# Kernel tuning notes

Measured on AMD Instinct MI355X. Metric: run time of the kernel, lower is better.

## Reference

```python
import jax, jax.numpy as jnp
import numpy as np


def setup_inputs() -> dict:
    key = jax.random.key(0)
    ks = jax.random.split(key, 5)
    B, N, d_emb, d_red = 8, 2048, 1024, 512
    x0 = jax.random.normal(ks[0], (B, N, d_emb), dtype=jnp.float32)
    x1 = jax.random.normal(ks[1], (B, N, d_emb), dtype=jnp.float32)
    x2 = jax.random.normal(ks[2], (B, N, d_emb), dtype=jnp.float32)
    Wq = jax.random.normal(ks[3], (d_emb, d_red), dtype=jnp.float32) * (1.0 / np.sqrt(d_emb))
    Wk = jax.random.normal(ks[4], (d_emb, d_red), dtype=jnp.float32) * (1.0 / np.sqrt(d_emb))
    bq = jnp.zeros((d_red,), dtype=jnp.float32)
    bk = jnp.zeros((d_red,), dtype=jnp.float32)
    return {"x0": x0, "x1": x1, "x2": x2, "Wq": Wq, "bq": bq, "Wk": Wk, "bk": bk}


def reference(x0, x1, x2, Wq, bq, Wk, bk):
    d_red = Wq.shape[1]
    # projections; NOTE: original code applies the K projection to x2 (v = self.k(x[2]))
    q = (x0 @ Wq + bq) * (1.0 / np.sqrt(d_red).astype(np.float32))
    k = x1 @ Wk + bk
    v = x2 @ Wk + bk
    scores = jnp.einsum('bqd,bkd->bqk', q, k)  # [B, N, N]
    N = scores.shape[-1]
    row = jnp.arange(N)[:, None]
    col = jnp.arange(N)[None, :]
    causal = jnp.where(col > row, -jnp.inf, 0.0).astype(scores.dtype)
    scores = scores + causal
    attn = jax.nn.softmax(scores, axis=-1)
    return jnp.einsum('bqk,bkd->bqd', attn, v)
```

## Files before the change

### kernel.cpp

```cpp
#include <hip/hip_runtime.h>
#include <hip/hip_bf16.h>
#include <math.h>


typedef __bf16 bf16_t;
typedef __attribute__((ext_vector_type(8))) __bf16 bf16x8;
typedef __attribute__((ext_vector_type(4))) __bf16 bf16x4;
typedef __attribute__((ext_vector_type(4))) float f32x4;

#define MFMA16(a, b, c) __builtin_amdgcn_mfma_f32_16x16x32_bf16((a), (b), (c), 0, 0, 0)

#define XSTR 72

__device__ __forceinline__ void stage16(const void* g, void* l) {
  __builtin_amdgcn_global_load_lds(
      (__attribute__((address_space(1))) void*)(uintptr_t)g,
      (__attribute__((address_space(3))) void*)l, 16, 0, 0);
}

#define PIPE_WAIT_MORE                          \
  {                                             \
    asm volatile("" ::: "memory");              \
    __builtin_amdgcn_s_waitcnt(0x0F74);         \
    __builtin_amdgcn_s_barrier();               \
    asm volatile("" ::: "memory");              \
  }
#define PIPE_WAIT_LAST                          \
  {                                             \
    asm volatile("" ::: "memory");              \
    __builtin_amdgcn_s_waitcnt(0x0F70);         \
    __builtin_amdgcn_s_barrier();               \
    asm volatile("" ::: "memory");              \
  }

#define PROJ_BAR_A                                    \
  {                                                   \
    asm volatile("s_waitcnt lgkmcnt(0)" ::: "memory"); \
    __builtin_amdgcn_s_barrier();                     \
    asm volatile("" ::: "memory");                    \
  }
#define PROJ_BAR_B                                    \
  {                                                   \
    __builtin_amdgcn_sched_barrier(0);                \
    __builtin_amdgcn_s_barrier();                     \
    asm volatile("" ::: "memory");                    \
  }

__global__ __launch_bounds__(256) void wt_kernel(const float* __restrict__ Wq,
                                                 const float* __restrict__ Wk,
                                                 bf16_t* __restrict__ Wtq,
                                                 bf16_t* __restrict__ Wtk) {
  __shared__ float tile[32][33];
  int bid = blockIdx.x;
  int mat = bid >> 9;
  int rem = bid & 511;
  int kt = rem >> 4, nt = rem & 15;
  int k0 = kt * 32, n0 = nt * 32;
  const float* src = mat ? Wk : Wq;
  bf16_t* dst = mat ? Wtk : Wtq;
  int t = threadIdx.x;
  int r = t >> 3, c4 = (t & 7) * 4;
  float4 v = *(const float4*)(src + (k0 + r) * 512 + n0 + c4);
  tile[r][c4 + 0] = v.x; tile[r][c4 + 1] = v.y;
  tile[r][c4 + 2] = v.z; tile[r][c4 + 3] = v.w;
  __syncthreads();
  bf16x4 o;
  o[0] = (bf16_t)tile[c4 + 0][r];
  o[1] = (bf16_t)tile[c4 + 1][r];
  o[2] = (bf16_t)tile[c4 + 2][r];
  o[3] = (bf16_t)tile[c4 + 3][r];
  *(bf16x4*)(dst + (n0 + r) * 1024 + k0 + c4) = o;
}

__global__ __launch_bounds__(256, 3) void proj_kernel(
    const float* __restrict__ x0, const float* __restrict__ x1, const float* __restrict__ x2,
    const bf16_t* __restrict__ Wtq, const bf16_t* __restrict__ Wtk,
    const float* __restrict__ bq, const float* __restrict__ bk,
    bf16_t* __restrict__ qo, bf16_t* __restrict__ ko, bf16_t* __restrict__ vT) {
  __shared__ __align__(16) bf16_t Xs[128 * XSTR];
  __shared__ __align__(16) bf16_t Ws[128 * XSTR];
  int bid = blockIdx.x;
  int xcd = bid & 7;
  int i5 = bid >> 3;
  int nblk = i5 & 3;
  int g = (i5 >> 2) * 8 + xcd;
  int mat = g >> 7;
  int mblk = g & 127;
  const float* xsrc = (mat == 0) ? x0 : ((mat == 1) ? x1 : x2);
  const bf16_t* wsrc = (mat == 0) ? Wtq : Wtk;
  int tid = threadIdx.x;
  int wave = tid >> 6, lane = tid & 63, lhi = lane >> 4, llo = lane & 15;

  f32x4 acc[2][8];
#pragma unroll
  for (int i = 0; i < 2; ++i)
#pragma unroll
    for (int j = 0; j < 8; ++j) acc[i][j] = (f32x4){0.f, 0.f, 0.f, 0.f};

  int xrow = tid >> 1, xseg = tid & 1;
  int wrow = tid >> 1, wseg = tid & 1;
  const float* xbase = xsrc + (size_t)(mblk * 128 + xrow) * 1024 + xseg * 32;
  const bf16_t* wbase = wsrc + (size_t)(nblk * 128 + wrow) * 1024 + wseg * 32;

  float4 nx[8];
  bf16x8 nw[4];

#pragma unroll
  for (int i = 0; i < 8; ++i) nx[i] = *(const float4*)(xbase + i * 4);
#pragma unroll
  for (int i = 0; i < 4; ++i) nw[i] = *(const bf16x8*)(wbase + i * 8);
  {
    bf16_t tmp[32];
#pragma unroll
    for (int i = 0; i < 8; ++i) {
      tmp[i * 4 + 0] = (bf16_t)nx[i].x; tmp[i * 4 + 1] = (bf16_t)nx[i].y;
      tmp[i * 4 + 2] = (bf16_t)nx[i].z; tmp[i * 4 + 3] = (bf16_t)nx[i].w;
    }
#pragma unroll
    for (int i = 0; i < 4; ++i)
      *(bf16x8*)(&Xs[xrow * XSTR + xseg * 32 + i * 8]) = *(bf16x8*)(&tmp[i * 8]);
#pragma unroll
    for (int i = 0; i < 4; ++i)
      *(bf16x8*)(&Ws[wrow * XSTR + wseg * 32 + i * 8]) = nw[i];
  }

  for (int kt = 0; kt < 16; ++kt) {
    PROJ_BAR_A;
    if (kt < 15) {
      int k0 = (kt + 1) * 64;
#pragma unroll
      for (int i = 0; i < 8; ++i) nx[i] = *(const float4*)(xbase + k0 + i * 4);
#pragma unroll
      for (int i = 0; i < 4; ++i) nw[i] = *(const bf16x8*)(wbase + k0 + i * 8);
    }
#pragma unroll
    for (int ks = 0; ks < 2; ++ks) {
      bf16x8 af[2], bfr[8];
#pragma unroll
      for (int mt = 0; mt < 2; ++mt)
        af[mt] = *(const bf16x8*)(&Xs[(wave * 32 + mt * 16 + llo) * XSTR + ks * 32 + lhi * 8]);
#pragma unroll
      for (int nt = 0; nt < 8; ++nt)
        bfr[nt] = *(const bf16x8*)(&Ws[(nt * 16 + llo) * XSTR + ks * 32 + lhi * 8]);
#pragma unroll
      for (int mt = 0; mt < 2; ++mt)
#pragma unroll
        for (int nt = 0; nt < 8; ++nt)
          acc[mt][nt] = MFMA16(af[mt], bfr[nt], acc[mt][nt]);
    }
    if (kt < 15) {
      PROJ_BAR_B;
      bf16_t tmp[32];
#pragma unroll
      for (int i = 0; i < 8; ++i) {
        tmp[i * 4 + 0] = (bf16_t)nx[i].x; tmp[i * 4 + 1] = (bf16_t)nx[i].y;
        tmp[i * 4 + 2] = (bf16_t)nx[i].z; tmp[i * 4 + 3] = (bf16_t)nx[i].w;
      }
#pragma unroll
      for (int i = 0; i < 4; ++i)
        *(bf16x8*)(&Xs[xrow * XSTR + xseg * 32 + i * 8]) = *(bf16x8*)(&tmp[i * 8]);
#pragma unroll
      for (int i = 0; i < 4; ++i)
        *(bf16x8*)(&Ws[wrow * XSTR + wseg * 32 + i * 8]) = nw[i];
    }
  }

  const float* bias = (mat == 0) ? bq : bk;
  float scale = (mat == 0) ? 0.044194173824159216f : 1.0f;
#pragma unroll
  for (int mt = 0; mt < 2; ++mt) {
#pragma unroll
    for (int nt = 0; nt < 8; ++nt) {
      int n = nblk * 128 + nt * 16 + llo;
      float bv = bias[n];
      int rowb = mblk * 128 + wave * 32 + mt * 16 + lhi * 4;
      float vals[4];
#pragma unroll
      for (int r = 0; r < 4; ++r) vals[r] = (acc[mt][nt][r] + bv) * scale;
      if (mat == 0) {
#pragma unroll
        for (int r = 0; r < 4; ++r) qo[(size_t)(rowb + r) * 512 + n] = (bf16_t)vals[r];
      } else if (mat == 1) {
#pragma unroll
        for (int r = 0; r < 4; ++r) ko[(size_t)(rowb + r) * 512 + n] = (bf16_t)vals[r];
      } else {
        int batch = rowb >> 11, tok = rowb & 2047;
        bf16x4 o;
        o[0] = (bf16_t)vals[0]; o[1] = (bf16_t)vals[1];
        o[2] = (bf16_t)vals[2]; o[3] = (bf16_t)vals[3];
        *(bf16x4*)(vT + (size_t)(batch * 512 + n) * 2048 + tok) = o;
      }
    }
  }
}

__device__ __forceinline__ void issueK(const bf16_t* kbase, int key0, int cd,
                                       bf16_t* buf, int wave, int lane) {
#pragma unroll
  for (int i = 0; i < 4; ++i) {
    int idx = wave * 256 + i * 64 + lane;
    int key = idx >> 4, p = idx & 15;
    int s = p ^ (key & 7);
    stage16(kbase + (size_t)(key0 + key) * 512 + cd * 128 + s * 8,
            buf + (size_t)(wave * 256 + i * 64) * 8);
  }
}
__device__ __forceinline__ void issueV(const bf16_t* vbase, int key0, int cv,
                                       bf16_t* buf, int wave, int lane) {
#pragma unroll
  for (int i = 0; i < 4; ++i) {
    int idx = wave * 256 + i * 64 + lane;
    int dl = idx >> 3, p = idx & 7;
    int s = p ^ (dl & 7);
    stage16(vbase + (size_t)(cv * 128 + dl) * 2048 + key0 + s * 8,
            buf + (size_t)(wave * 256 + i * 64) * 8);
  }
}

__global__ __launch_bounds__(256, 2) void attn_kernel(
    const bf16_t* __restrict__ qg, const bf16_t* __restrict__ kg,
    const bf16_t* __restrict__ vTg, float* __restrict__ out,
    bf16_t* __restrict__ Opart, float* __restrict__ msum, float* __restrict__ lsum) {
  __shared__ __align__(16) bf16_t Pipe[3][8192];
  __shared__ __align__(16) bf16_t Plds[4][16 * XSTR];

  int bid = blockIdx.x;
  int b = bid & 7, jj = bid >> 3;
  int t = 31, base = 0, n = 6;
  for (;;) {
    int nt_ = (t + 6) / 6;
    if (jj < base + nt_) { n = nt_; break; }
    base += nt_; --t;
  }
  int c = jj - base;
  int kbs = t + 1;
  int csz = (kbs + n - 1) / n;
  int kb_lo = c * csz;
  int kb_hi = min(kbs, kb_lo + csz);
  int q0 = t * 64;

  int tid = threadIdx.x;
  int wave = tid >> 6, lane = tid & 63, lhi = lane >> 4, llo = lane & 15;
  bf16_t* Pb = &Plds[wave][0];

  const bf16_t* kbase = kg + ((size_t)b << 11) * 512;
  const bf16_t* vbase = vTg + ((size_t)b << 9) * 2048;

  int bc = 0;
  issueK(kbase, kb_lo * 64, 0, &Pipe[0][0], wave, lane);

  const bf16_t* qrowp = qg + (size_t)((b << 11) + q0 + wave * 16 + llo) * 512;
  bf16x8 qf[16];
#pragma unroll
  for (int kk = 0; kk < 16; ++kk)
    qf[kk] = *(const bf16x8*)(qrowp + kk * 32 + lhi * 8);

  f32x4 Of[32];
#pragma unroll
  for (int i = 0; i < 32; ++i) Of[i] = (f32x4){0.f, 0.f, 0.f, 0.f};
  float m_i[4] = {-INFINITY, -INFINITY, -INFINITY, -INFINITY};
  float l_i[4] = {0.f, 0.f, 0.f, 0.f};

  for (int kb = kb_lo; kb < kb_hi; ++kb) {
    int key0 = kb * 64;
    f32x4 sf[4];
#pragma unroll
    for (int nt = 0; nt < 4; ++nt) sf[nt] = (f32x4){0.f, 0.f, 0.f, 0.f};

#pragma unroll
    for (int cd = 0; cd < 4; ++cd) {
      int nb = (bc + 1 == 3) ? 0 : bc + 1;
      if (cd < 3) issueK(kbase, key0, cd + 1, &Pipe[nb][0], wave, lane);
      else        issueV(vbase, key0, 0, &Pipe[nb][0], wave, lane);
      PIPE_WAIT_MORE;
      const bf16_t* bufc = &Pipe[bc][0];
#pragma unroll
      for (int kkl = 0; kkl < 4; ++kkl) {
#pragma unroll
        for (int nt = 0; nt < 4; ++nt) {
          bf16x8 kf = *(const bf16x8*)(bufc + (nt * 16 + llo) * 128 +
                                       (((kkl * 4 + lhi) ^ (llo & 7)) * 8));
          sf[nt] = MFMA16(qf[cd * 4 + kkl], kf, sf[nt]);
        }
      }
      bc = nb;
    }

    if (kb == t) {
#pragma unroll
      for (int nt = 0; nt < 4; ++nt) {
        int kloc = nt * 16 + llo;
#pragma unroll
        for (int r = 0; r < 4; ++r)
          if (kloc > wave * 16 + lhi * 4 + r) sf[nt][r] = -INFINITY;
      }
    }
    float vm[4];
#pragma unroll
    for (int r = 0; r < 4; ++r) {
      vm[r] = fmaxf(fmaxf(sf[0][r], sf[1][r]), fmaxf(sf[2][r], sf[3][r]));
      vm[r] = fmaxf(vm[r], __shfl_xor(vm[r], 1, 64));
      vm[r] = fmaxf(vm[r], __shfl_xor(vm[r], 2, 64));
      vm[r] = fmaxf(vm[r], __shfl_xor(vm[r], 4, 64));
      vm[r] = fmaxf(vm[r], __shfl_xor(vm[r], 8, 64));
    }
    float alpha[4];
    int resc = 0;
#pragma unroll
    for (int r = 0; r < 4; ++r) {
      float mn = fmaxf(m_i[r], vm[r]);
      alpha[r] = __expf(m_i[r] - mn);
      m_i[r] = mn;
      resc |= (alpha[r] < 1.0f) ? 1 : 0;
    }
#pragma unroll
    for (int r = 0; r < 4; ++r) {
      float ps = 0.f;
#pragma unroll
      for (int nt = 0; nt < 4; ++nt) {
        float p = __expf(sf[nt][r] - m_i[r]);
        ps += p;
        Pb[(lhi * 4 + r) * XSTR + nt * 16 + llo] = (bf16_t)p;
      }
      l_i[r] = alpha[r] * l_i[r] + ps;
    }
    if (__any(resc)) {
#pragma unroll
      for (int i = 0; i < 32; ++i)
#pragma unroll
        for (int r = 0; r < 4; ++r) Of[i][r] *= alpha[r];
    }

#pragma unroll
    for (int cv = 0; cv < 4; ++cv) {
      int nb = (bc + 1 == 3) ? 0 : bc + 1;
      bool last = (cv == 3) && (kb + 1 >= kb_hi);
      if (cv < 3) issueV(vbase, key0, cv + 1, &Pipe[nb][0], wave, lane);
      else if (!last) issueK(kbase, key0 + 64, 0, &Pipe[nb][0], wave, lane);
      if (last) PIPE_WAIT_LAST else PIPE_WAIT_MORE;
      const bf16_t* bufc = &Pipe[bc][0];
#pragma unroll
      for (int ks = 0; ks < 2; ++ks) {
        bf16x8 pa = *(const bf16x8*)(&Pb[llo * XSTR + ks * 32 + lhi * 8]);
#pragma unroll
        for (int ntl = 0; ntl < 8; ++ntl) {
          bf16x8 bv = *(const bf16x8*)(bufc + (ntl * 16 + llo) * 64 +
                                       (((ks * 4 + lhi) ^ (llo & 7)) * 8));
          Of[cv * 8 + ntl] = MFMA16(pa, bv, Of[cv * 8 + ntl]);
        }
      }
      bc = nb;
    }
  }

#pragma unroll
  for (int r = 0; r < 4; ++r) {
    l_i[r] += __shfl_xor(l_i[r], 1, 64);
    l_i[r] += __shfl_xor(l_i[r], 2, 64);
    l_i[r] += __shfl_xor(l_i[r], 4, 64);
    l_i[r] += __shfl_xor(l_i[r], 8, 64);
  }

  if (n == 1) {
    float linv[4];
#pragma unroll
    for (int r = 0; r < 4; ++r) linv[r] = 1.0f / l_i[r];
    float* ob = out + (size_t)((b << 11) + q0 + wave * 16) * 512;
#pragma unroll
    for (int i = 0; i < 32; ++i) {
      int dcol = ((i >> 3) << 7) + ((i & 7) << 4) + llo;
#pragma unroll
      for (int r = 0; r < 4; ++r)
        ob[(size_t)(lhi * 4 + r) * 512 + dcol] = Of[i][r] * linv[r];
    }
  } else {
    bf16_t* op = Opart + (size_t)bid * (64 * 512) + (size_t)(wave * 16) * 512;
#pragma unroll
    for (int i = 0; i < 32; ++i) {
      int dcol = ((i >> 3) << 7) + ((i & 7) << 4) + llo;
#pragma unroll
      for (int r = 0; r < 4; ++r)
        op[(size_t)(lhi * 4 + r) * 512 + dcol] = (bf16_t)Of[i][r];
    }
    if (llo == 0) {
#pragma unroll
      for (int r = 0; r < 4; ++r) {
        msum[bid * 64 + wave * 16 + lhi * 4 + r] = m_i[r];
        lsum[bid * 64 + wave * 16 + lhi * 4 + r] = l_i[r];
      }
    }
  }
}

__global__ __launch_bounds__(256) void merge_kernel(const bf16_t* __restrict__ Opart,
                                                    const float* __restrict__ msum,
                                                    const float* __restrict__ lsum,
                                                    float* __restrict__ out) {
  int idx = blockIdx.x * 256 + threadIdx.x;
  int d = idx & 511;
  int rg = idx >> 9;
  int b = rg / 1664;
  int rr = rg - b * 1664;
  int t = 6 + (rr >> 6), row = rr & 63;
  int base = 0;
  for (int s = 31; s > t; --s) base += (s + 6) / 6;
  int n = (t + 6) / 6;
  float M = -INFINITY;
  for (int c2 = 0; c2 < n; ++c2)
    M = fmaxf(M, msum[((base + c2) * 8 + b) * 64 + row]);
  float denom = 0.f, acc = 0.f;
  for (int c2 = 0; c2 < n; ++c2) {
    int j = (base + c2) * 8 + b;
    float a = __expf(msum[j * 64 + row] - M);
    denom += a * lsum[j * 64 + row];
    acc += a * (float)Opart[(size_t)j * (64 * 512) + row * 512 + d];
  }
  out[(size_t)((b << 11) + (t << 6) + row) * 512 + d] = acc / denom;
}

extern "C" void kernel_launch(void* const* d_in, const int* in_sizes, int n_in,
                              void* d_out, int out_size, void* d_ws, size_t ws_size,
                              hipStream_t stream) {
  (void)in_sizes; (void)n_in; (void)out_size; (void)ws_size;
  const float* x0 = (const float*)d_in[0];
  const float* x1 = (const float*)d_in[1];
  const float* x2 = (const float*)d_in[2];
  const float* Wq = (const float*)d_in[3];
  const float* bq = (const float*)d_in[4];
  const float* Wk = (const float*)d_in[5];
  const float* bk = (const float*)d_in[6];
  float* out = (float*)d_out;
  char* ws = (char*)d_ws;
  const size_t MB = 1ull << 20;
  bf16_t* Wtq = (bf16_t*)(ws + 0 * MB);
  bf16_t* Wtk = (bf16_t*)(ws + 1 * MB);
  bf16_t* qw  = (bf16_t*)(ws + 2 * MB);
  bf16_t* kw  = (bf16_t*)(ws + 18 * MB);
  bf16_t* vT  = (bf16_t*)(ws + 34 * MB);
  float* msum = (float*)(ws + 50 * MB);
  float* lsum = (float*)(ws + 50 * MB + (512 << 10));
  bf16_t* Opart = (bf16_t*)(ws + 51 * MB);

  hipLaunchKernelGGL(wt_kernel, dim3(1024), dim3(256), 0, stream, Wq, Wk, Wtq, Wtk);
  hipLaunchKernelGGL(proj_kernel, dim3(1536), dim3(256), 0, stream,
                     x0, x1, x2, Wtq, Wtk, bq, bk, qw, kw, vT);
  hipLaunchKernelGGL(attn_kernel, dim3(816), dim3(256), 0, stream,
                     qw, kw, vT, out, Opart, msum, lsum);
  hipLaunchKernelGGL(merge_kernel, dim3(26624), dim3(256), 0, stream,
                     Opart, msum, lsum, out);
}
```

Before: 540.3 us.

## Deepen K/V LDS staging pipeline to four buffers with two chunks in flight

Raises the shared-memory staging ring from three to four 16KB buffers and prefetches two chunks ahead instead of one, waiting on vmcnt(8) so two async global→LDS loads stay outstanding during each MFMA block. It also raises wave priority around the MFMA loops with s_setprio. This targets global load latency exposed at each barrier, but adds 16KB of LDS per block, which may cut occupancy below the two blocks per CU the launch bounds ask for.

```diff
diff --git a/kernel.cpp b/kernel.cpp
--- a/kernel.cpp
+++ b/kernel.cpp
@@ -18,14 +18,21 @@
       (__attribute__((address_space(3))) void*)l, 16, 0, 0);
 }
 
-#define PIPE_WAIT_MORE                          \
+#define PIPE_VM8                                \
+  {                                             \
+    asm volatile("" ::: "memory");              \
+    __builtin_amdgcn_s_waitcnt(0x0F78);         \
+    __builtin_amdgcn_s_barrier();               \
+    asm volatile("" ::: "memory");              \
+  }
+#define PIPE_VM4                                \
   {                                             \
     asm volatile("" ::: "memory");              \
     __builtin_amdgcn_s_waitcnt(0x0F74);         \
     __builtin_amdgcn_s_barrier();               \
     asm volatile("" ::: "memory");              \
   }
-#define PIPE_WAIT_LAST                          \
+#define PIPE_VM0                                \
   {                                             \
     asm volatile("" ::: "memory");              \
     __builtin_amdgcn_s_waitcnt(0x0F70);         \
@@ -221,7 +228,7 @@
     const bf16_t* __restrict__ qg, const bf16_t* __restrict__ kg,
     const bf16_t* __restrict__ vTg, float* __restrict__ out,
     bf16_t* __restrict__ Opart, float* __restrict__ msum, float* __restrict__ lsum) {
-  __shared__ __align__(16) bf16_t Pipe[3][8192];
+  __shared__ __align__(16) bf16_t Pipe[4][8192];
   __shared__ __align__(16) bf16_t Plds[4][16 * XSTR];
 
   int bid = blockIdx.x;
@@ -247,7 +254,9 @@
   const bf16_t* vbase = vTg + ((size_t)b << 9) * 2048;
 
   int bc = 0;
+  int ib = 2;
   issueK(kbase, kb_lo * 64, 0, &Pipe[0][0], wave, lane);
+  issueK(kbase, kb_lo * 64, 1, &Pipe[1][0], wave, lane);
 
   const bf16_t* qrowp = qg + (size_t)((b << 11) + q0 + wave * 16 + llo) * 512;
   bf16x8 qf[16];
@@ -263,17 +272,19 @@
 
   for (int kb = kb_lo; kb < kb_hi; ++kb) {
     int key0 = kb * 64;
+    bool more = (kb + 1 < kb_hi);
     f32x4 sf[4];
 #pragma unroll
     for (int nt = 0; nt < 4; ++nt) sf[nt] = (f32x4){0.f, 0.f, 0.f, 0.f};
 
 #pragma unroll
     for (int cd = 0; cd < 4; ++cd) {
-      int nb = (bc + 1 == 3) ? 0 : bc + 1;
-      if (cd < 3) issueK(kbase, key0, cd + 1, &Pipe[nb][0], wave, lane);
-      else        issueV(vbase, key0, 0, &Pipe[nb][0], wave, lane);
-      PIPE_WAIT_MORE;
+      if (cd < 2) issueK(kbase, key0, cd + 2, &Pipe[ib][0], wave, lane);
+      else        issueV(vbase, key0, cd - 2, &Pipe[ib][0], wave, lane);
+      ib = (ib + 1) & 3;
+      PIPE_VM8;
       const bf16_t* bufc = &Pipe[bc][0];
+      __builtin_amdgcn_s_setprio(1);
 #pragma unroll
       for (int kkl = 0; kkl < 4; ++kkl) {
 #pragma unroll
@@ -283,7 +294,8 @@
           sf[nt] = MFMA16(qf[cd * 4 + kkl], kf, sf[nt]);
         }
       }
-      bc = nb;
+      __builtin_amdgcn_s_setprio(0);
+      bc = (bc + 1) & 3;
     }
 
     if (kb == t) {
@@ -333,12 +345,21 @@
 
 #pragma unroll
     for (int cv = 0; cv < 4; ++cv) {
-      int nb = (bc + 1 == 3) ? 0 : bc + 1;
-      bool last = (cv == 3) && (kb + 1 >= kb_hi);
-      if (cv < 3) issueV(vbase, key0, cv + 1, &Pipe[nb][0], wave, lane);
-      else if (!last) issueK(kbase, key0 + 64, 0, &Pipe[nb][0], wave, lane);
-      if (last) PIPE_WAIT_LAST else PIPE_WAIT_MORE;
+      if (cv < 2) {
+        issueV(vbase, key0, cv + 2, &Pipe[ib][0], wave, lane);
+        ib = (ib + 1) & 3;
+        PIPE_VM8;
+      } else if (more) {
+        issueK(kbase, key0 + 64, cv - 2, &Pipe[ib][0], wave, lane);
+        ib = (ib + 1) & 3;
+        PIPE_VM8;
+      } else if (cv == 2) {
+        PIPE_VM4;
+      } else {
+        PIPE_VM0;
+      }
       const bf16_t* bufc = &Pipe[bc][0];
+      __builtin_amdgcn_s_setprio(1);
 #pragma unroll
       for (int ks = 0; ks < 2; ++ks) {
         bf16x8 pa = *(const bf16x8*)(&Pb[llo * XSTR + ks * 32 + lhi * 8]);
@@ -349,7 +370,8 @@
           Of[cv * 8 + ntl] = MFMA16(pa, bv, Of[cv * 8 + ntl]);
         }
       }
-      bc = nb;
+      __builtin_amdgcn_s_setprio(0);
+      bc = (bc + 1) & 3;
     }
   }
 
```

New measurement: 567.3 us. 1.05x slower.

## Replace triple-buffered quarter-chunk pipeline with double-buffered half-chunk phases

Applied to the files above, without the earlier changes.

The K/V staging pipeline changes from three 16KB buffers cycling over eight quarter-chunks per key block to two 32KB buffers, each holding two quarter-chunks. Each phase issues the next half-block load right after a full vmcnt(0) wait and barrier. Barriers per key block drop from eight to four, cutting sync overhead. In exchange the loads are less finely overlapped, since each phase waits for all outstanding loads, and LDS use grows from 48KB to 64KB per block, which may affect two-block occupancy.

```diff
diff --git a/kernel.cpp b/kernel.cpp
--- a/kernel.cpp
+++ b/kernel.cpp
@@ -18,14 +18,7 @@
       (__attribute__((address_space(3))) void*)l, 16, 0, 0);
 }
 
-#define PIPE_WAIT_MORE                          \
-  {                                             \
-    asm volatile("" ::: "memory");              \
-    __builtin_amdgcn_s_waitcnt(0x0F74);         \
-    __builtin_amdgcn_s_barrier();               \
-    asm volatile("" ::: "memory");              \
-  }
-#define PIPE_WAIT_LAST                          \
+#define PHASE_SYNC                              \
   {                                             \
     asm volatile("" ::: "memory");              \
     __builtin_amdgcn_s_waitcnt(0x0F70);         \
@@ -221,7 +214,7 @@
     const bf16_t* __restrict__ qg, const bf16_t* __restrict__ kg,
     const bf16_t* __restrict__ vTg, float* __restrict__ out,
     bf16_t* __restrict__ Opart, float* __restrict__ msum, float* __restrict__ lsum) {
-  __shared__ __align__(16) bf16_t Pipe[3][8192];
+  __shared__ __align__(16) bf16_t Pipe[2][16384];
   __shared__ __align__(16) bf16_t Plds[4][16 * XSTR];
 
   int bid = blockIdx.x;
@@ -246,8 +239,9 @@
   const bf16_t* kbase = kg + ((size_t)b << 11) * 512;
   const bf16_t* vbase = vTg + ((size_t)b << 9) * 2048;
 
-  int bc = 0;
+  int p = 0;
   issueK(kbase, kb_lo * 64, 0, &Pipe[0][0], wave, lane);
+  issueK(kbase, kb_lo * 64, 1, &Pipe[0][8192], wave, lane);
 
   const bf16_t* qrowp = qg + (size_t)((b << 11) + q0 + wave * 16 + llo) * 512;
   bf16x8 qf[16];
@@ -263,27 +257,36 @@
 
   for (int kb = kb_lo; kb < kb_hi; ++kb) {
     int key0 = kb * 64;
+    bool more = (kb + 1 < kb_hi);
     f32x4 sf[4];
 #pragma unroll
     for (int nt = 0; nt < 4; ++nt) sf[nt] = (f32x4){0.f, 0.f, 0.f, 0.f};
 
 #pragma unroll
-    for (int cd = 0; cd < 4; ++cd) {
-      int nb = (bc + 1 == 3) ? 0 : bc + 1;
-      if (cd < 3) issueK(kbase, key0, cd + 1, &Pipe[nb][0], wave, lane);
-      else        issueV(vbase, key0, 0, &Pipe[nb][0], wave, lane);
-      PIPE_WAIT_MORE;
-      const bf16_t* bufc = &Pipe[bc][0];
-#pragma unroll
-      for (int kkl = 0; kkl < 4; ++kkl) {
-#pragma unroll
-        for (int nt = 0; nt < 4; ++nt) {
-          bf16x8 kf = *(const bf16x8*)(bufc + (nt * 16 + llo) * 128 +
-                                       (((kkl * 4 + lhi) ^ (llo & 7)) * 8));
-          sf[nt] = MFMA16(qf[cd * 4 + kkl], kf, sf[nt]);
+    for (int h = 0; h < 2; ++h) {
+      PHASE_SYNC;
+      if (h == 0) {
+        issueK(kbase, key0, 2, &Pipe[p ^ 1][0], wave, lane);
+        issueK(kbase, key0, 3, &Pipe[p ^ 1][8192], wave, lane);
+      } else {
+        issueV(vbase, key0, 0, &Pipe[p ^ 1][0], wave, lane);
+        issueV(vbase, key0, 1, &Pipe[p ^ 1][8192], wave, lane);
+      }
+#pragma unroll
+      for (int sub = 0; sub < 2; ++sub) {
+        const bf16_t* bufc = &Pipe[p][sub * 8192];
+        int cd = h * 2 + sub;
+#pragma unroll
+        for (int kkl = 0; kkl < 4; ++kkl) {
+#pragma unroll
+          for (int nt = 0; nt < 4; ++nt) {
+            bf16x8 kf = *(const bf16x8*)(bufc + (nt * 16 + llo) * 128 +
+                                         (((kkl * 4 + lhi) ^ (llo & 7)) * 8));
+            sf[nt] = MFMA16(qf[cd * 4 + kkl], kf, sf[nt]);
+          }
         }
       }
-      bc = nb;
+      p ^= 1;
     }
 
     if (kb == t) {
@@ -318,9 +321,9 @@
       float ps = 0.f;
 #pragma unroll
       for (int nt = 0; nt < 4; ++nt) {
-        float p = __expf(sf[nt][r] - m_i[r]);
-        ps += p;
-        Pb[(lhi * 4 + r) * XSTR + nt * 16 + llo] = (bf16_t)p;
+        float p2 = __expf(sf[nt][r] - m_i[r]);
+        ps += p2;
+        Pb[(lhi * 4 + r) * XSTR + nt * 16 + llo] = (bf16_t)p2;
       }
       l_i[r] = alpha[r] * l_i[r] + ps;
     }
@@ -332,24 +335,31 @@
     }
 
 #pragma unroll
-    for (int cv = 0; cv < 4; ++cv) {
-      int nb = (bc + 1 == 3) ? 0 : bc + 1;
-      bool last = (cv == 3) && (kb + 1 >= kb_hi);
-      if (cv < 3) issueV(vbase, key0, cv + 1, &Pipe[nb][0], wave, lane);
-      else if (!last) issueK(kbase, key0 + 64, 0, &Pipe[nb][0], wave, lane);
-      if (last) PIPE_WAIT_LAST else PIPE_WAIT_MORE;
-      const bf16_t* bufc = &Pipe[bc][0];
-#pragma unroll
-      for (int ks = 0; ks < 2; ++ks) {
-        bf16x8 pa = *(const bf16x8*)(&Pb[llo * XSTR + ks * 32 + lhi * 8]);
-#pragma unroll
-        for (int ntl = 0; ntl < 8; ++ntl) {
-          bf16x8 bv = *(const bf16x8*)(bufc + (ntl * 16 + llo) * 64 +
-                                       (((ks * 4 + lhi) ^ (llo & 7)) * 8));
-          Of[cv * 8 + ntl] = MFMA16(pa, bv, Of[cv * 8 + ntl]);
+    for (int h = 0; h < 2; ++h) {
+      PHASE_SYNC;
+      if (h == 0) {
+        issueV(vbase, key0, 2, &Pipe[p ^ 1][0], wave, lane);
+        issueV(vbase, key0, 3, &Pipe[p ^ 1][8192], wave, lane);
+      } else if (more) {
+        issueK(kbase, key0 + 64, 0, &Pipe[p ^ 1][0], wave, lane);
+        issueK(kbase, key0 + 64, 1, &Pipe[p ^ 1][8192], wave, lane);
+      }
+#pragma unroll
+      for (int sub = 0; sub < 2; ++sub) {
+        const bf16_t* bufc = &Pipe[p][sub * 8192];
+        int cv = h * 2 + sub;
+#pragma unroll
+        for (int ks = 0; ks < 2; ++ks) {
+          bf16x8 pa = *(const bf16x8*)(&Pb[llo * XSTR + ks * 32 + lhi * 8]);
+#pragma unroll
+          for (int ntl = 0; ntl < 8; ++ntl) {
+            bf16x8 bv = *(const bf16x8*)(bufc + (ntl * 16 + llo) * 64 +
+                                         (((ks * 4 + lhi) ^ (llo & 7)) * 8));
+            Of[cv * 8 + ntl] = MFMA16(pa, bv, Of[cv * 8 + ntl]);
+          }
         }
       }
-      bc = nb;
+      p ^= 1;
     }
   }
 
```

Result: slower. 555.2 us (+2.8%).

## Halve attention pipeline stage size to 64-wide chunks and use nontemporal stores

Applied to the files above, without the earlier changes.

Splits each K and V tile load into eight 64-column stages instead of four 128-column stages. This halves the LDS ring buffer (3x8KB instead of 3x16KB) and adjusts the waitcnt to match two loads per stage, aiming for finer-grained overlap and less LDS per block. Output and partial stores, and the merge loads, now use nontemporal hints. The cost is twice as many barriers per key block, each covering less MFMA work.

```diff
diff --git a/kernel.cpp b/kernel.cpp
--- a/kernel.cpp
+++ b/kernel.cpp
@@ -18,14 +18,14 @@
       (__attribute__((address_space(3))) void*)l, 16, 0, 0);
 }
 
-#define PIPE_WAIT_MORE                          \
+#define PW_MORE                                 \
   {                                             \
     asm volatile("" ::: "memory");              \
-    __builtin_amdgcn_s_waitcnt(0x0F74);         \
+    __builtin_amdgcn_s_waitcnt(0x0F72);         \
     __builtin_amdgcn_s_barrier();               \
     asm volatile("" ::: "memory");              \
   }
-#define PIPE_WAIT_LAST                          \
+#define PW_LAST                                 \
   {                                             \
     asm volatile("" ::: "memory");              \
     __builtin_amdgcn_s_waitcnt(0x0F70);         \
@@ -194,26 +194,26 @@
   }
 }
 
-__device__ __forceinline__ void issueK(const bf16_t* kbase, int key0, int cd,
-                                       bf16_t* buf, int wave, int lane) {
-#pragma unroll
-  for (int i = 0; i < 4; ++i) {
-    int idx = wave * 256 + i * 64 + lane;
-    int key = idx >> 4, p = idx & 15;
+__device__ __forceinline__ void issueK8(const bf16_t* kbase, int key0, int cd,
+                                        bf16_t* buf, int wave, int lane) {
+#pragma unroll
+  for (int i = 0; i < 2; ++i) {
+    int idx = wave * 128 + i * 64 + lane;
+    int key = idx >> 3, p = idx & 7;
     int s = p ^ (key & 7);
-    stage16(kbase + (size_t)(key0 + key) * 512 + cd * 128 + s * 8,
-            buf + (size_t)(wave * 256 + i * 64) * 8);
-  }
-}
-__device__ __forceinline__ void issueV(const bf16_t* vbase, int key0, int cv,
-                                       bf16_t* buf, int wave, int lane) {
-#pragma unroll
-  for (int i = 0; i < 4; ++i) {
-    int idx = wave * 256 + i * 64 + lane;
+    stage16(kbase + (size_t)(key0 + key) * 512 + cd * 64 + s * 8,
+            buf + (size_t)(wave * 128 + i * 64) * 8);
+  }
+}
+__device__ __forceinline__ void issueV8(const bf16_t* vbase, int key0, int cv,
+                                        bf16_t* buf, int wave, int lane) {
+#pragma unroll
+  for (int i = 0; i < 2; ++i) {
+    int idx = wave * 128 + i * 64 + lane;
     int dl = idx >> 3, p = idx & 7;
     int s = p ^ (dl & 7);
-    stage16(vbase + (size_t)(cv * 128 + dl) * 2048 + key0 + s * 8,
-            buf + (size_t)(wave * 256 + i * 64) * 8);
+    stage16(vbase + (size_t)(cv * 64 + dl) * 2048 + key0 + s * 8,
+            buf + (size_t)(wave * 128 + i * 64) * 8);
   }
 }
 
@@ -221,7 +221,7 @@
     const bf16_t* __restrict__ qg, const bf16_t* __restrict__ kg,
     const bf16_t* __restrict__ vTg, float* __restrict__ out,
     bf16_t* __restrict__ Opart, float* __restrict__ msum, float* __restrict__ lsum) {
-  __shared__ __align__(16) bf16_t Pipe[3][8192];
+  __shared__ __align__(16) bf16_t Pipe[3][4096];
   __shared__ __align__(16) bf16_t Plds[4][16 * XSTR];
 
   int bid = blockIdx.x;
@@ -247,7 +247,7 @@
   const bf16_t* vbase = vTg + ((size_t)b << 9) * 2048;
 
   int bc = 0;
-  issueK(kbase, kb_lo * 64, 0, &Pipe[0][0], wave, lane);
+  issueK8(kbase, kb_lo * 64, 0, &Pipe[0][0], wave, lane);
 
   const bf16_t* qrowp = qg + (size_t)((b << 11) + q0 + wave * 16 + llo) * 512;
   bf16x8 qf[16];
@@ -263,24 +263,25 @@
 
   for (int kb = kb_lo; kb < kb_hi; ++kb) {
     int key0 = kb * 64;
+    bool more = (kb + 1 < kb_hi);
     f32x4 sf[4];
 #pragma unroll
     for (int nt = 0; nt < 4; ++nt) sf[nt] = (f32x4){0.f, 0.f, 0.f, 0.f};
 
 #pragma unroll
-    for (int cd = 0; cd < 4; ++cd) {
+    for (int cd = 0; cd < 8; ++cd) {
       int nb = (bc + 1 == 3) ? 0 : bc + 1;
-      if (cd < 3) issueK(kbase, key0, cd + 1, &Pipe[nb][0], wave, lane);
-      else        issueV(vbase, key0, 0, &Pipe[nb][0], wave, lane);
-      PIPE_WAIT_MORE;
+      if (cd < 7) issueK8(kbase, key0, cd + 1, &Pipe[nb][0], wave, lane);
+      else        issueV8(vbase, key0, 0, &Pipe[nb][0], wave, lane);
+      PW_MORE;
       const bf16_t* bufc = &Pipe[bc][0];
 #pragma unroll
-      for (int kkl = 0; kkl < 4; ++kkl) {
+      for (int kkl = 0; kkl < 2; ++kkl) {
 #pragma unroll
         for (int nt = 0; nt < 4; ++nt) {
-          bf16x8 kf = *(const bf16x8*)(bufc + (nt * 16 + llo) * 128 +
+          bf16x8 kf = *(const bf16x8*)(bufc + (nt * 16 + llo) * 64 +
                                        (((kkl * 4 + lhi) ^ (llo & 7)) * 8));
-          sf[nt] = MFMA16(qf[cd * 4 + kkl], kf, sf[nt]);
+          sf[nt] = MFMA16(qf[cd * 2 + kkl], kf, sf[nt]);
         }
       }
       bc = nb;
@@ -318,9 +319,9 @@
       float ps = 0.f;
 #pragma unroll
       for (int nt = 0; nt < 4; ++nt) {
-        float p = __expf(sf[nt][r] - m_i[r]);
-        ps += p;
-        Pb[(lhi * 4 + r) * XSTR + nt * 16 + llo] = (bf16_t)p;
+        float p2 = __expf(sf[nt][r] - m_i[r]);
+        ps += p2;
+        Pb[(lhi * 4 + r) * XSTR + nt * 16 + llo] = (bf16_t)p2;
       }
       l_i[r] = alpha[r] * l_i[r] + ps;
     }
@@ -332,21 +333,21 @@
     }
 
 #pragma unroll
-    for (int cv = 0; cv < 4; ++cv) {
+    for (int cv = 0; cv < 8; ++cv) {
       int nb = (bc + 1 == 3) ? 0 : bc + 1;
-      bool last = (cv == 3) && (kb + 1 >= kb_hi);
-      if (cv < 3) issueV(vbase, key0, cv + 1, &Pipe[nb][0], wave, lane);
-      else if (!last) issueK(kbase, key0 + 64, 0, &Pipe[nb][0], wave, lane);
-      if (last) PIPE_WAIT_LAST else PIPE_WAIT_MORE;
+      bool last = (cv == 7) && !more;
+      if (cv < 7)      issueV8(vbase, key0, cv + 1, &Pipe[nb][0], wave, lane);
+      else if (more)   issueK8(kbase, key0 + 64, 0, &Pipe[nb][0], wave, lane);
+      if (last) PW_LAST else PW_MORE;
       const bf16_t* bufc = &Pipe[bc][0];
 #pragma unroll
       for (int ks = 0; ks < 2; ++ks) {
         bf16x8 pa = *(const bf16x8*)(&Pb[llo * XSTR + ks * 32 + lhi * 8]);
 #pragma unroll
-        for (int ntl = 0; ntl < 8; ++ntl) {
+        for (int ntl = 0; ntl < 4; ++ntl) {
           bf16x8 bv = *(const bf16x8*)(bufc + (ntl * 16 + llo) * 64 +
                                        (((ks * 4 + lhi) ^ (llo & 7)) * 8));
-          Of[cv * 8 + ntl] = MFMA16(pa, bv, Of[cv * 8 + ntl]);
+          Of[cv * 4 + ntl] = MFMA16(pa, bv, Of[cv * 4 + ntl]);
         }
       }
       bc = nb;
@@ -368,19 +369,21 @@
     float* ob = out + (size_t)((b << 11) + q0 + wave * 16) * 512;
 #pragma unroll
     for (int i = 0; i < 32; ++i) {
-      int dcol = ((i >> 3) << 7) + ((i & 7) << 4) + llo;
+      int dcol = i * 16 + llo;
 #pragma unroll
       for (int r = 0; r < 4; ++r)
-        ob[(size_t)(lhi * 4 + r) * 512 + dcol] = Of[i][r] * linv[r];
+        __builtin_nontemporal_store(Of[i][r] * linv[r],
+                                    &ob[(size_t)(lhi * 4 + r) * 512 + dcol]);
     }
   } else {
     bf16_t* op = Opart + (size_t)bid * (64 * 512) + (size_t)(wave * 16) * 512;
 #pragma unroll
     for (int i = 0; i < 32; ++i) {
-      int dcol = ((i >> 3) << 7) + ((i & 7) << 4) + llo;
+      int dcol = i * 16 + llo;
 #pragma unroll
       for (int r = 0; r < 4; ++r)
-        op[(size_t)(lhi * 4 + r) * 512 + dcol] = (bf16_t)Of[i][r];
+        __builtin_nontemporal_store((bf16_t)Of[i][r],
+                                    &op[(size_t)(lhi * 4 + r) * 512 + dcol]);
     }
     if (llo == 0) {
 #pragma unroll
@@ -413,9 +416,11 @@
     int j = (base + c2) * 8 + b;
     float a = __expf(msum[j * 64 + row] - M);
     denom += a * lsum[j * 64 + row];
-    acc += a * (float)Opart[(size_t)j * (64 * 512) + row * 512 + d];
-  }
-  out[(size_t)((b << 11) + (t << 6) + row) * 512 + d] = acc / denom;
+    bf16_t ov = __builtin_nontemporal_load(&Opart[(size_t)j * (64 * 512) + row * 512 + d]);
+    acc += a * (float)ov;
+  }
+  __builtin_nontemporal_store(acc / denom,
+                              &out[(size_t)((b << 11) + (t << 6) + row) * 512 + d]);
 }
 
 extern "C" void kernel_launch(void* const* d_in, const int* in_sizes, int n_in,
```

Measured after the change: 527.0 us. 2.5% less time.
